# Kernel tuning notes

Hardware: AMD Instinct MI355X
Metric: run time of the kernel (lower is better)

The kernel has to match this reference:

```python
import jax, jax.numpy as jnp
import numpy as np

B, N, C, M, OUT = 4, 256, 32, 4, 64


def _uniform(k, shape, fan_in):
    s = 1.0 / np.sqrt(fan_in)
    return jax.random.uniform(k, shape, jnp.float32, -s, s)


def setup_inputs() -> dict:
    key = jax.random.key(0)
    ks = jax.random.split(key, 11)
    return {
        "x": jax.random.normal(ks[0], (B, N, N, C), jnp.float32),
        # Neighborhood / SnConv2to1 linears (in=C, out=M neighborhood channels)
        "w1_nb": _uniform(ks[1], (3 * C, M), 3 * C),
        "b1_nb": _uniform(ks[2], (M,), 3 * C),
        "w0_nb": _uniform(ks[3], (2 * C, M), 2 * C),
        "b0_nb": _uniform(ks[4], (M,), 2 * C),
        # SnConv2 linears (in channels = M*C after neighborhood product)
        "w2d": _uniform(ks[5], (2 * M * C, OUT), 2 * M * C),
        "b2d": _uniform(ks[6], (OUT,), 2 * M * C),
        "w1d": _uniform(ks[7], (3 * M * C, OUT), 3 * M * C),
        "b1d": _uniform(ks[8], (OUT,), 3 * M * C),
        "w0d": _uniform(ks[9], (2 * M * C, OUT), 2 * M * C),
        "b0d": _uniform(ks[10], (OUT,), 2 * M * C),
    }


def _contractions(x):
    # x: [B, n, n, c]; mask=None, reduction='mean' path of _get_contractions
    n = x.shape[1]
    rowsum = x.sum(axis=1) / n                      # [B, n, c]
    colsum = x.sum(axis=2) / n                      # [B, n, c]
    diag = jnp.diagonal(x, axis1=1, axis2=2)        # [B, c, n]
    rowcolsum = x.sum(axis=(1, 2)) / (n * n)        # [B, c]
    diag_sum = diag.sum(axis=-1) / n                # [B, c]  (/= sqrt(n^2))
    diag = jnp.moveaxis(diag, -1, 1)                # move_from_end -> [B, n, c]
    return rowsum, colsum, diag, rowcolsum, diag_sum


def reference(x, w1_nb, b1_nb, w0_nb, b0_nb, w2d, b2d, w1d, b1d, w0d, b0d):
    # ---- Neighborhood: SnConv2to1 -> sigmoid ----
    rs, cs, dg, rcs, ds = _contractions(x)
    obj1 = jnp.concatenate([rs, cs, dg], axis=-1)             # [B, n, 3C]
    obj0 = jnp.concatenate([rcs, ds], axis=-1)                # [B, 2C]
    node = obj1 @ w1_nb + b1_nb + (obj0 @ w0_nb + b0_nb)[:, None, :]
    neighbs = jax.nn.sigmoid(node)                            # [B, n, M]
    # ---- _neighbor_elementwise_product ----
    expanded = neighbs[:, None, :, :] * neighbs[:, :, None, :]  # [B, n, n, M]
    # channel_product: outer product over channel dims, collapsed to M*C
    xl = (expanded[..., :, None] * x[..., None, :]).reshape(B, N, N, M * C)
    # ---- SnConv2 on the localized tensor ----
    rs2, cs2, dg2, rcs2, ds2 = _contractions(xl)
    obj2d = jnp.concatenate([xl, jnp.swapaxes(xl, 1, 2)], axis=-1)  # [B,n,n,2MC]
    obj1d = jnp.concatenate([rs2, cs2, dg2], axis=-1)               # [B,n,3MC]
    obj0d = jnp.concatenate([rcs2, ds2], axis=-1)                   # [B,2MC]
    out = (obj2d @ w2d + b2d
           + (obj1d @ w1d + b1d)[:, None, :, :]
           + (obj0d @ w0d + b0d)[:, None, None, :])                 # [B,n,n,OUT]
    return out
```

## Files before the change

### kernel.cpp

```cpp
#include <hip/hip_runtime.h>
#include <math.h>

#define Bv 4
#define Nv 256
#define Cv 32
#define Mv 4
#define OUTv 64
#define MCv (Mv*Cv)

typedef _Float16 h8 __attribute__((ext_vector_type(8)));
typedef _Float16 h4 __attribute__((ext_vector_type(4)));
typedef float f4 __attribute__((ext_vector_type(4)));

__device__ __align__(16) float g_rs  [Bv * Nv * Cv];
__device__ __align__(16) float g_cs  [Bv * Nv * Cv];
__device__ __align__(16) float g_dgx [Bv * Nv * Cv];
__device__ __align__(16) float g_nb  [Bv * Nv * Mv];
__device__ __align__(16) float g_S1  [Bv * Nv * MCv];
__device__ __align__(16) float g_S2  [Bv * Nv * MCv];
__device__ __align__(16) float g_rcs2[Bv * MCv];
__device__ __align__(16) float g_ds2 [Bv * MCv];
__device__ __align__(16) float g_t0g [Bv * OUTv];
__device__ __align__(16) float g_addv[Bv * Nv * OUTv];
__device__ __align__(16) _Float16 g_wfrag[8 * 4 * 64 * 8];

__global__ void k_wpackz(const float* __restrict__ w2d) {
    int t = threadIdx.x;
    int r = blockIdx.x;
    if (r == 8) {
        if (t < 128) ((float4*)g_rcs2)[t] = {0.f,0.f,0.f,0.f};
        else         ((float4*)g_ds2)[t - 128] = {0.f,0.f,0.f,0.f};
        return;
    }
    int fi = r * 256 + t;
    int s = fi >> 8, q = (fi >> 6) & 3, lane = fi & 63;
    int k0 = s * 32 + ((lane >> 4) << 3);
    int o = q * 16 + (lane & 15);
    #pragma unroll
    for (int jj = 0; jj < 8; jj++)
        g_wfrag[fi * 8 + jj] = (_Float16)w2d[(size_t)(k0 + jj) * OUTv + o];
}

__global__ __launch_bounds__(256) void k_contract1(const float* __restrict__ x) {
    int bx = blockIdx.x, b = blockIdx.y;
    int t = threadIdx.x, c4 = t & 7, sub = t >> 3;
    const float4* xb4 = (const float4*)(x + (size_t)b * Nv * Nv * Cv);
    __shared__ float red[32][36];
    float4 acc = {0.f,0.f,0.f,0.f};
    if (bx < Nv) {
        int n = bx;
        for (int i = sub; i < Nv; i += 32) {
            float4 v = xb4[((size_t)i * Nv + n) * 8 + c4];
            acc.x += v.x; acc.y += v.y; acc.z += v.z; acc.w += v.w;
        }
        red[sub][c4*4+0] = acc.x; red[sub][c4*4+1] = acc.y;
        red[sub][c4*4+2] = acc.z; red[sub][c4*4+3] = acc.w;
        __syncthreads();
        if (t < 32) {
            float s = 0.f;
            #pragma unroll
            for (int k = 0; k < 32; k++) s += red[k][t];
            g_rs[(b * Nv + n) * Cv + t] = s * (1.0f / Nv);
        }
        if (t < 8) ((float4*)g_dgx)[(b * Nv + n) * 8 + t] = xb4[((size_t)n * Nv + n) * 8 + t];
    } else {
        int n = bx - Nv;
        for (int j = sub; j < Nv; j += 32) {
            float4 v = xb4[((size_t)n * Nv + j) * 8 + c4];
            acc.x += v.x; acc.y += v.y; acc.z += v.z; acc.w += v.w;
        }
        red[sub][c4*4+0] = acc.x; red[sub][c4*4+1] = acc.y;
        red[sub][c4*4+2] = acc.z; red[sub][c4*4+3] = acc.w;
        __syncthreads();
        if (t < 32) {
            float s = 0.f;
            #pragma unroll
            for (int k = 0; k < 32; k++) s += red[k][t];
            g_cs[(b * Nv + n) * Cv + t] = s * (1.0f / Nv);
        }
    }
}

__global__ void k_neighb(const float* __restrict__ w1, const float* __restrict__ b1,
                         const float* __restrict__ w0, const float* __restrict__ b0) {
    int b = blockIdx.x, t = threadIdx.x;
    int c = t & 31, sub = t >> 5;
    float ar = 0.f, ad = 0.f;
    for (int n = sub; n < Nv; n += 8) {
        ar += g_rs[(b * Nv + n) * Cv + c];
        ad += g_dgx[(b * Nv + n) * Cv + c];
    }
    __shared__ float red[8][64];
    __shared__ float obj0[64];
    __shared__ float t0nb[4];
    red[sub][c] = ar;
    red[sub][32 + c] = ad;
    __syncthreads();
    if (t < 64) {
        float s = 0.f;
        #pragma unroll
        for (int k = 0; k < 8; k++) s += red[k][t];
        obj0[t] = s * (1.0f / Nv);
    }
    __syncthreads();
    if (t < 4) {
        float v = b0[t];
        for (int k = 0; k < 2 * Cv; k++) v += obj0[k] * w0[k * Mv + t];
        t0nb[t] = v;
    }
    __syncthreads();
    int n = t;
    float node[4];
    #pragma unroll
    for (int m = 0; m < 4; m++) node[m] = t0nb[m] + b1[m];
    for (int cc = 0; cc < Cv; cc++) {
        float r = g_rs[(b * Nv + n) * Cv + cc];
        float s = g_cs[(b * Nv + n) * Cv + cc];
        float d = g_dgx[(b * Nv + n) * Cv + cc];
        #pragma unroll
        for (int m = 0; m < 4; m++)
            node[m] += r * w1[cc * Mv + m] + s * w1[(Cv + cc) * Mv + m] + d * w1[(2 * Cv + cc) * Mv + m];
    }
    #pragma unroll
    for (int m = 0; m < 4; m++)
        g_nb[(b * Nv + n) * Mv + m] = 1.0f / (1.0f + expf(-node[m]));
}

__global__ __launch_bounds__(256) void k_wsum(const float* __restrict__ x) {
    int bx = blockIdx.x, b = blockIdx.y;
    int t = threadIdx.x, c4 = t & 7, sub = t >> 3;
    __shared__ __align__(16) float4 nbl[Nv];
    if (t < Nv) nbl[t] = ((const float4*)(g_nb + (size_t)b * Nv * Mv))[t];
    __syncthreads();
    const float4* xb4 = (const float4*)(x + (size_t)b * Nv * Nv * Cv);
    float4 a[4];
    #pragma unroll
    for (int m = 0; m < 4; m++) a[m] = {0.f,0.f,0.f,0.f};
    __shared__ float red[32][132];
    if (bx < Nv) {
        int n = bx;
        for (int i = sub; i < Nv; i += 32) {
            float4 v = xb4[((size_t)i * Nv + n) * 8 + c4];
            float4 nv = nbl[i];
            a[0].x += nv.x*v.x; a[0].y += nv.x*v.y; a[0].z += nv.x*v.z; a[0].w += nv.x*v.w;
            a[1].x += nv.y*v.x; a[1].y += nv.y*v.y; a[1].z += nv.y*v.z; a[1].w += nv.y*v.w;
            a[2].x += nv.z*v.x; a[2].y += nv.z*v.y; a[2].z += nv.z*v.z; a[2].w += nv.z*v.w;
            a[3].x += nv.w*v.x; a[3].y += nv.w*v.y; a[3].z += nv.w*v.z; a[3].w += nv.w*v.w;
        }
        #pragma unroll
        for (int m = 0; m < 4; m++) {
            red[sub][m*32 + c4*4+0] = a[m].x; red[sub][m*32 + c4*4+1] = a[m].y;
            red[sub][m*32 + c4*4+2] = a[m].z; red[sub][m*32 + c4*4+3] = a[m].w;
        }
        __syncthreads();
        if (t < 128) {
            float s = 0.f;
            #pragma unroll
            for (int k = 0; k < 32; k++) s += red[k][t];
            g_S1[(size_t)(b * Nv + n) * MCv + t] = s;
            int m = t >> 5, c = t & 31;
            float nv = ((const float*)&nbl[n])[m];
            atomicAdd(&g_rcs2[b * MCv + t], nv * s);
            atomicAdd(&g_ds2 [b * MCv + t], nv * nv * g_dgx[(b * Nv + n) * Cv + c]);
        }
    } else {
        int n = bx - Nv;
        for (int j = sub; j < Nv; j += 32) {
            float4 v = xb4[((size_t)n * Nv + j) * 8 + c4];
            float4 nv = nbl[j];
            a[0].x += nv.x*v.x; a[0].y += nv.x*v.y; a[0].z += nv.x*v.z; a[0].w += nv.x*v.w;
            a[1].x += nv.y*v.x; a[1].y += nv.y*v.y; a[1].z += nv.y*v.z; a[1].w += nv.y*v.w;
            a[2].x += nv.z*v.x; a[2].y += nv.z*v.y; a[2].z += nv.z*v.z; a[2].w += nv.z*v.w;
            a[3].x += nv.w*v.x; a[3].y += nv.w*v.y; a[3].z += nv.w*v.z; a[3].w += nv.w*v.w;
        }
        #pragma unroll
        for (int m = 0; m < 4; m++) {
            red[sub][m*32 + c4*4+0] = a[m].x; red[sub][m*32 + c4*4+1] = a[m].y;
            red[sub][m*32 + c4*4+2] = a[m].z; red[sub][m*32 + c4*4+3] = a[m].w;
        }
        __syncthreads();
        if (t < 128) {
            float s = 0.f;
            #pragma unroll
            for (int k = 0; k < 32; k++) s += red[k][t];
            g_S2[(size_t)(b * Nv + n) * MCv + t] = s;
        }
    }
}

__global__ void k_t0(const float* __restrict__ w0d, const float* __restrict__ b0d) {
    int b = blockIdx.x, t = threadIdx.x;
    __shared__ float rc[MCv], ds[MCv];
    rc[t] = g_rcs2[b * MCv + t] * (1.0f / ((float)Nv * Nv));
    ds[t] = g_ds2 [b * MCv + t] * (1.0f / Nv);
    __syncthreads();
    if (t < OUTv) {
        float v = b0d[t];
        for (int k = 0; k < MCv; k++)
            v += rc[k] * w0d[k * OUTv + t] + ds[k] * w0d[(MCv + k) * OUTv + t];
        g_t0g[b * OUTv + t] = v;
    }
}

__global__ __launch_bounds__(256) void k_add(const float* __restrict__ w1d,
                                             const float* __restrict__ b1d,
                                             const float* __restrict__ b2d) {
    int b = blockIdx.y, n = blockIdx.x;
    int t = threadIdx.x, o = t & 63, ks = t >> 6;
    __shared__ float red[4][64];
    const float invN = 1.0f / Nv;
    float nv = g_nb[(b * Nv + n) * Mv + ks];
    float f = nv * invN, d2 = nv * nv;
    const float* S1r = g_S1 + (size_t)(b * Nv + n) * MCv + ks * 32;
    const float* S2r = g_S2 + (size_t)(b * Nv + n) * MCv + ks * 32;
    const float* dgr = g_dgx + (size_t)(b * Nv + n) * Cv;
    float acc = 0.f;
    #pragma unroll 8
    for (int c = 0; c < 32; c++) {
        int mc = ks * 32 + c;
        acc += f * S1r[c] * w1d[(size_t)mc * OUTv + o]
             + f * S2r[c] * w1d[(size_t)(MCv + mc) * OUTv + o]
             + d2 * dgr[c] * w1d[(size_t)(2 * MCv + mc) * OUTv + o];
    }
    red[ks][o] = acc;
    __syncthreads();
    if (t < 64) {
        float v = red[0][t] + red[1][t] + red[2][t] + red[3][t]
                + b1d[t] + b2d[t] + g_t0g[b * OUTv + t];
        g_addv[(size_t)(b * Nv + n) * OUTv + t] = v;
    }
}

#define XPAD 40
__global__ __launch_bounds__(256) void k_main(const float* __restrict__ x,
                                              float* __restrict__ out) {
    int jt = blockIdx.x, i = blockIdx.y, b = blockIdx.z;
    int j0 = jt * 128;
    int t = threadIdx.x;
    int lane = t & 63, w = t >> 6;
    int rowA = lane & 15, quad = lane >> 4;

    __shared__ __align__(16) _Float16 Wl[8 * 4 * 64 * 8];
    __shared__ __align__(16) _Float16 Xt[128 * XPAD];
    __shared__ __align__(16) _Float16 Xb[128 * XPAD];

    {
        const float4* src = (const float4*)g_wfrag;
        float4* dst = (float4*)Wl;
        #pragma unroll
        for (int r = 0; r < 8; r++) dst[r * 256 + t] = src[r * 256 + t];
    }
    {
        const float4* x4 = (const float4*)x;
        #pragma unroll
        for (int r = 0; r < 4; r++) {
            int idx = r * 256 + t;
            int j = idx >> 3, c4 = idx & 7;
            float4 v = x4[((size_t)(b * Nv + i) * Nv + j0 + j) * 8 + c4];
            h4 hv; hv[0] = (_Float16)v.x; hv[1] = (_Float16)v.y;
            hv[2] = (_Float16)v.z; hv[3] = (_Float16)v.w;
            *(h4*)&Xt[j * XPAD + c4 * 4] = hv;
            float4 u = x4[((size_t)(b * Nv + j0 + j) * Nv + i) * 8 + c4];
            h4 hu; hu[0] = (_Float16)u.x; hu[1] = (_Float16)u.y;
            hu[2] = (_Float16)u.z; hu[3] = (_Float16)u.w;
            *(h4*)&Xb[j * XPAD + c4 * 4] = hu;
        }
    }
    int jl1 = w * 32 + rowA, jl2 = jl1 + 16;
    _Float16 e1h[4], e2h[4];
    {
        const float* ni = g_nb + (size_t)(b * Nv + i) * Mv;
        const float* n1 = g_nb + (size_t)(b * Nv + j0 + jl1) * Mv;
        const float* n2 = g_nb + (size_t)(b * Nv + j0 + jl2) * Mv;
        #pragma unroll
        for (int m = 0; m < 4; m++) {
            e1h[m] = (_Float16)(ni[m] * n1[m]);
            e2h[m] = (_Float16)(ni[m] * n2[m]);
        }
    }
    __syncthreads();

    f4 acc[2][4];
    #pragma unroll
    for (int js = 0; js < 2; js++)
        #pragma unroll
        for (int q = 0; q < 4; q++) acc[js][q] = {0.f, 0.f, 0.f, 0.f};

    const h8* Wf = (const h8*)Wl;
    #pragma unroll
    for (int part = 0; part < 2; part++) {
        const _Float16* X = part ? Xb : Xt;
        h8 xv1 = *(const h8*)&X[jl1 * XPAD + quad * 8];
        h8 xv2 = *(const h8*)&X[jl2 * XPAD + quad * 8];
        #pragma unroll
        for (int m = 0; m < 4; m++) {
            h8 a1 = xv1 * e1h[m];
            h8 a2 = xv2 * e2h[m];
            int s = part * 4 + m;
            #pragma unroll
            for (int q = 0; q < 4; q++) {
                h8 bf = Wf[(s * 4 + q) * 64 + lane];
                acc[0][q] = __builtin_amdgcn_mfma_f32_16x16x32_f16(a1, bf, acc[0][q], 0, 0, 0);
                acc[1][q] = __builtin_amdgcn_mfma_f32_16x16x32_f16(a2, bf, acc[1][q], 0, 0, 0);
            }
        }
    }
    #pragma unroll
    for (int js = 0; js < 2; js++) {
        int jbase = j0 + w * 32 + js * 16 + quad * 4;
        #pragma unroll
        for (int q = 0; q < 4; q++) {
            int o = q * 16 + rowA;
            #pragma unroll
            for (int r = 0; r < 4; r++) {
                int j = jbase + r;
                float v = acc[js][q][r] + g_addv[(size_t)(b * Nv + j) * OUTv + o];
                out[(((size_t)(b * Nv + i)) * Nv + j) * OUTv + o] = v;
            }
        }
    }
}

extern "C" void kernel_launch(void* const* d_in, const int* in_sizes, int n_in,
                              void* d_out, int out_size, void* d_ws, size_t ws_size,
                              hipStream_t stream) {
    const float* x     = (const float*)d_in[0];
    const float* w1_nb = (const float*)d_in[1];
    const float* b1_nb = (const float*)d_in[2];
    const float* w0_nb = (const float*)d_in[3];
    const float* b0_nb = (const float*)d_in[4];
    const float* w2d   = (const float*)d_in[5];
    const float* b2d   = (const float*)d_in[6];
    const float* w1d   = (const float*)d_in[7];
    const float* b1d   = (const float*)d_in[8];
    const float* w0d   = (const float*)d_in[9];
    const float* b0d   = (const float*)d_in[10];
    float* out = (float*)d_out;
    (void)d_ws; (void)ws_size;

    hipLaunchKernelGGL(k_wpackz, dim3(9), dim3(256), 0, stream, w2d);
    hipLaunchKernelGGL(k_contract1, dim3(2 * Nv, Bv), dim3(256), 0, stream, x);
    hipLaunchKernelGGL(k_neighb, dim3(Bv), dim3(256), 0, stream,
                       w1_nb, b1_nb, w0_nb, b0_nb);
    hipLaunchKernelGGL(k_wsum, dim3(2 * Nv, Bv), dim3(256), 0, stream, x);
    hipLaunchKernelGGL(k_t0, dim3(Bv), dim3(128), 0, stream, w0d, b0d);
    hipLaunchKernelGGL(k_add, dim3(Nv, Bv), dim3(256), 0, stream,
                       w1d, b1d, b2d);
    hipLaunchKernelGGL(k_main, dim3(2, Nv, Bv), dim3(256), 0, stream, x, out);
}
```

Baseline: 185.1 us.

## Fuse small kernels, parallelize neighborhood, tile main kernel over multiple rows

The obj0 reduction moves into k_contract1 via atomics. k_neighb is spread over more blocks with a split channel reduction, and k_t0 is folded into k_add. k_main now handles ITILE rows of i per block, so the weight-fragment LDS staging, the addv row loads and the neighbour loads are reused across rows, and outputs use nontemporal stores. This cuts launch count and redundant per-block setup, at the cost of fewer blocks in k_main, float atomics that make summation order nondeterministic, and a redundant w0d computation in every k_add block.

```diff
diff --git a/kernel.cpp b/kernel.cpp
--- a/kernel.cpp
+++ b/kernel.cpp
@@ -7,6 +7,7 @@
 #define Mv 4
 #define OUTv 64
 #define MCv (Mv*Cv)
+#define ITILE 4
 
 typedef _Float16 h8 __attribute__((ext_vector_type(8)));
 typedef _Float16 h4 __attribute__((ext_vector_type(4)));
@@ -18,9 +19,9 @@
 __device__ __align__(16) float g_nb  [Bv * Nv * Mv];
 __device__ __align__(16) float g_S1  [Bv * Nv * MCv];
 __device__ __align__(16) float g_S2  [Bv * Nv * MCv];
+__device__ __align__(16) float g_obj0[Bv * 64];
 __device__ __align__(16) float g_rcs2[Bv * MCv];
 __device__ __align__(16) float g_ds2 [Bv * MCv];
-__device__ __align__(16) float g_t0g [Bv * OUTv];
 __device__ __align__(16) float g_addv[Bv * Nv * OUTv];
 __device__ __align__(16) _Float16 g_wfrag[8 * 4 * 64 * 8];
 
@@ -30,6 +31,7 @@
     if (r == 8) {
         if (t < 128) ((float4*)g_rcs2)[t] = {0.f,0.f,0.f,0.f};
         else         ((float4*)g_ds2)[t - 128] = {0.f,0.f,0.f,0.f};
+        if (t < 64)  ((float4*)g_obj0)[t] = {0.f,0.f,0.f,0.f};
         return;
     }
     int fi = r * 256 + t;
@@ -47,6 +49,7 @@
     const float4* xb4 = (const float4*)(x + (size_t)b * Nv * Nv * Cv);
     __shared__ float red[32][36];
     float4 acc = {0.f,0.f,0.f,0.f};
+    const float invN = 1.0f / Nv;
     if (bx < Nv) {
         int n = bx;
         for (int i = sub; i < Nv; i += 32) {
@@ -60,9 +63,18 @@
             float s = 0.f;
             #pragma unroll
             for (int k = 0; k < 32; k++) s += red[k][t];
-            g_rs[(b * Nv + n) * Cv + t] = s * (1.0f / Nv);
-        }
-        if (t < 8) ((float4*)g_dgx)[(b * Nv + n) * 8 + t] = xb4[((size_t)n * Nv + n) * 8 + t];
+            s *= invN;
+            g_rs[(b * Nv + n) * Cv + t] = s;
+            atomicAdd(&g_obj0[b * 64 + t], s * invN);
+        }
+        if (t < 8) {
+            float4 v = xb4[((size_t)n * Nv + n) * 8 + t];
+            ((float4*)g_dgx)[(b * Nv + n) * 8 + t] = v;
+            atomicAdd(&g_obj0[b * 64 + 32 + t*4 + 0], v.x * invN);
+            atomicAdd(&g_obj0[b * 64 + 32 + t*4 + 1], v.y * invN);
+            atomicAdd(&g_obj0[b * 64 + 32 + t*4 + 2], v.z * invN);
+            atomicAdd(&g_obj0[b * 64 + 32 + t*4 + 3], v.w * invN);
+        }
     } else {
         int n = bx - Nv;
         for (int j = sub; j < Nv; j += 32) {
@@ -76,54 +88,53 @@
             float s = 0.f;
             #pragma unroll
             for (int k = 0; k < 32; k++) s += red[k][t];
-            g_cs[(b * Nv + n) * Cv + t] = s * (1.0f / Nv);
-        }
-    }
-}
-
-__global__ void k_neighb(const float* __restrict__ w1, const float* __restrict__ b1,
-                         const float* __restrict__ w0, const float* __restrict__ b0) {
-    int b = blockIdx.x, t = threadIdx.x;
-    int c = t & 31, sub = t >> 5;
-    float ar = 0.f, ad = 0.f;
-    for (int n = sub; n < Nv; n += 8) {
-        ar += g_rs[(b * Nv + n) * Cv + c];
-        ad += g_dgx[(b * Nv + n) * Cv + c];
-    }
-    __shared__ float red[8][64];
-    __shared__ float obj0[64];
-    __shared__ float t0nb[4];
-    red[sub][c] = ar;
-    red[sub][32 + c] = ad;
-    __syncthreads();
-    if (t < 64) {
-        float s = 0.f;
-        #pragma unroll
-        for (int k = 0; k < 8; k++) s += red[k][t];
-        obj0[t] = s * (1.0f / Nv);
-    }
+            g_cs[(b * Nv + n) * Cv + t] = s * invN;
+        }
+    }
+}
+
+__global__ __launch_bounds__(256) void k_neighb(const float* __restrict__ w1,
+                                                const float* __restrict__ b1,
+                                                const float* __restrict__ w0,
+                                                const float* __restrict__ b0) {
+    int ng = blockIdx.x, b = blockIdx.y;
+    int t = threadIdx.x;
+    __shared__ float obj0[64], t0nb[4];
+    if (t < 64) obj0[t] = g_obj0[b * 64 + t];
     __syncthreads();
     if (t < 4) {
         float v = b0[t];
-        for (int k = 0; k < 2 * Cv; k++) v += obj0[k] * w0[k * Mv + t];
+        for (int k = 0; k < 64; k++) v += obj0[k] * w0[k * Mv + t];
         t0nb[t] = v;
     }
+    int n = ng * 64 + (t >> 2), part = t & 3;
+    float node[4] = {0.f, 0.f, 0.f, 0.f};
+    const float* rsr = g_rs  + (size_t)(b * Nv + n) * Cv;
+    const float* csr = g_cs  + (size_t)(b * Nv + n) * Cv;
+    const float* dgr = g_dgx + (size_t)(b * Nv + n) * Cv;
+    #pragma unroll
+    for (int q = 0; q < 8; q++) {
+        int cc = part * 8 + q;
+        float r = rsr[cc], s = csr[cc], d = dgr[cc];
+        #pragma unroll
+        for (int m = 0; m < 4; m++)
+            node[m] += r * w1[cc * Mv + m] + s * w1[(Cv + cc) * Mv + m]
+                     + d * w1[(2 * Cv + cc) * Mv + m];
+    }
+    __shared__ float red[256][4];
+    #pragma unroll
+    for (int m = 0; m < 4; m++) red[t][m] = node[m];
     __syncthreads();
-    int n = t;
-    float node[4];
-    #pragma unroll
-    for (int m = 0; m < 4; m++) node[m] = t0nb[m] + b1[m];
-    for (int cc = 0; cc < Cv; cc++) {
-        float r = g_rs[(b * Nv + n) * Cv + cc];
-        float s = g_cs[(b * Nv + n) * Cv + cc];
-        float d = g_dgx[(b * Nv + n) * Cv + cc];
-        #pragma unroll
-        for (int m = 0; m < 4; m++)
-            node[m] += r * w1[cc * Mv + m] + s * w1[(Cv + cc) * Mv + m] + d * w1[(2 * Cv + cc) * Mv + m];
-    }
-    #pragma unroll
-    for (int m = 0; m < 4; m++)
-        g_nb[(b * Nv + n) * Mv + m] = 1.0f / (1.0f + expf(-node[m]));
+    if (part == 0) {
+        float4 o4;
+        #pragma unroll
+        for (int m = 0; m < 4; m++) {
+            float v = t0nb[m] + b1[m]
+                    + red[t][m] + red[t+1][m] + red[t+2][m] + red[t+3][m];
+            ((float*)&o4)[m] = 1.0f / (1.0f + expf(-v));
+        }
+        ((float4*)g_nb)[b * Nv + n] = o4;
+    }
 }
 
 __global__ __launch_bounds__(256) void k_wsum(const float* __restrict__ x) {
@@ -188,33 +199,29 @@
     }
 }
 
-__global__ void k_t0(const float* __restrict__ w0d, const float* __restrict__ b0d) {
-    int b = blockIdx.x, t = threadIdx.x;
-    __shared__ float rc[MCv], ds[MCv];
-    rc[t] = g_rcs2[b * MCv + t] * (1.0f / ((float)Nv * Nv));
-    ds[t] = g_ds2 [b * MCv + t] * (1.0f / Nv);
-    __syncthreads();
-    if (t < OUTv) {
-        float v = b0d[t];
-        for (int k = 0; k < MCv; k++)
-            v += rc[k] * w0d[k * OUTv + t] + ds[k] * w0d[(MCv + k) * OUTv + t];
-        g_t0g[b * OUTv + t] = v;
-    }
-}
-
 __global__ __launch_bounds__(256) void k_add(const float* __restrict__ w1d,
                                              const float* __restrict__ b1d,
-                                             const float* __restrict__ b2d) {
+                                             const float* __restrict__ b2d,
+                                             const float* __restrict__ w0d,
+                                             const float* __restrict__ b0d) {
     int b = blockIdx.y, n = blockIdx.x;
     int t = threadIdx.x, o = t & 63, ks = t >> 6;
     __shared__ float red[4][64];
     const float invN = 1.0f / Nv;
+    const float invN2 = 1.0f / ((float)Nv * Nv);
+    float acc = 0.f;
+    #pragma unroll 8
+    for (int c = 0; c < 32; c++) {
+        int k = ks * 32 + c;
+        float rc = g_rcs2[b * MCv + k] * invN2;
+        float dv = g_ds2 [b * MCv + k] * invN;
+        acc += rc * w0d[(size_t)k * OUTv + o] + dv * w0d[(size_t)(MCv + k) * OUTv + o];
+    }
     float nv = g_nb[(b * Nv + n) * Mv + ks];
     float f = nv * invN, d2 = nv * nv;
     const float* S1r = g_S1 + (size_t)(b * Nv + n) * MCv + ks * 32;
     const float* S2r = g_S2 + (size_t)(b * Nv + n) * MCv + ks * 32;
     const float* dgr = g_dgx + (size_t)(b * Nv + n) * Cv;
-    float acc = 0.f;
     #pragma unroll 8
     for (int c = 0; c < 32; c++) {
         int mc = ks * 32 + c;
@@ -226,7 +233,7 @@
     __syncthreads();
     if (t < 64) {
         float v = red[0][t] + red[1][t] + red[2][t] + red[3][t]
-                + b1d[t] + b2d[t] + g_t0g[b * OUTv + t];
+                + b1d[t] + b2d[t] + b0d[t];
         g_addv[(size_t)(b * Nv + n) * OUTv + t] = v;
     }
 }
@@ -234,8 +241,8 @@
 #define XPAD 40
 __global__ __launch_bounds__(256) void k_main(const float* __restrict__ x,
                                               float* __restrict__ out) {
-    int jt = blockIdx.x, i = blockIdx.y, b = blockIdx.z;
-    int j0 = jt * 128;
+    int jt = blockIdx.x, ib = blockIdx.y, b = blockIdx.z;
+    int j0 = jt * 128, i0 = ib * ITILE;
     int t = threadIdx.x;
     int lane = t & 63, w = t >> 6;
     int rowA = lane & 15, quad = lane >> 4;
@@ -250,8 +257,24 @@
         #pragma unroll
         for (int r = 0; r < 8; r++) dst[r * 256 + t] = src[r * 256 + t];
     }
-    {
-        const float4* x4 = (const float4*)x;
+    int jl1 = w * 32 + rowA, jl2 = jl1 + 16;
+    float av[2][4][4];
+    #pragma unroll
+    for (int js = 0; js < 2; js++) {
+        int jb = j0 + w * 32 + js * 16 + quad * 4;
+        #pragma unroll
+        for (int q = 0; q < 4; q++)
+            #pragma unroll
+            for (int r = 0; r < 4; r++)
+                av[js][q][r] = g_addv[(size_t)(b * Nv + jb + r) * OUTv + q * 16 + rowA];
+    }
+    float4 nj1 = ((const float4*)g_nb)[b * Nv + j0 + jl1];
+    float4 nj2 = ((const float4*)g_nb)[b * Nv + j0 + jl2];
+    const float4* x4 = (const float4*)x;
+    const h8* Wf = (const h8*)Wl;
+
+    for (int ii = 0; ii < ITILE; ii++) {
+        int i = i0 + ii;
         #pragma unroll
         for (int r = 0; r < 4; r++) {
             int idx = r * 256 + t;
@@ -265,59 +288,55 @@
             hu[2] = (_Float16)u.z; hu[3] = (_Float16)u.w;
             *(h4*)&Xb[j * XPAD + c4 * 4] = hu;
         }
-    }
-    int jl1 = w * 32 + rowA, jl2 = jl1 + 16;
-    _Float16 e1h[4], e2h[4];
-    {
-        const float* ni = g_nb + (size_t)(b * Nv + i) * Mv;
-        const float* n1 = g_nb + (size_t)(b * Nv + j0 + jl1) * Mv;
-        const float* n2 = g_nb + (size_t)(b * Nv + j0 + jl2) * Mv;
+        float4 ni = ((const float4*)g_nb)[b * Nv + i];
+        _Float16 e1h[4], e2h[4];
         #pragma unroll
         for (int m = 0; m < 4; m++) {
-            e1h[m] = (_Float16)(ni[m] * n1[m]);
-            e2h[m] = (_Float16)(ni[m] * n2[m]);
-        }
-    }
-    __syncthreads();
-
-    f4 acc[2][4];
-    #pragma unroll
-    for (int js = 0; js < 2; js++)
-        #pragma unroll
-        for (int q = 0; q < 4; q++) acc[js][q] = {0.f, 0.f, 0.f, 0.f};
-
-    const h8* Wf = (const h8*)Wl;
-    #pragma unroll
-    for (int part = 0; part < 2; part++) {
-        const _Float16* X = part ? Xb : Xt;
-        h8 xv1 = *(const h8*)&X[jl1 * XPAD + quad * 8];
-        h8 xv2 = *(const h8*)&X[jl2 * XPAD + quad * 8];
-        #pragma unroll
-        for (int m = 0; m < 4; m++) {
-            h8 a1 = xv1 * e1h[m];
-            h8 a2 = xv2 * e2h[m];
-            int s = part * 4 + m;
+            e1h[m] = (_Float16)(((const float*)&ni)[m] * ((const float*)&nj1)[m]);
+            e2h[m] = (_Float16)(((const float*)&ni)[m] * ((const float*)&nj2)[m]);
+        }
+        __syncthreads();
+
+        f4 acc[2][4];
+        #pragma unroll
+        for (int js = 0; js < 2; js++)
+            #pragma unroll
+            for (int q = 0; q < 4; q++) acc[js][q] = {0.f, 0.f, 0.f, 0.f};
+
+        #pragma unroll
+        for (int part = 0; part < 2; part++) {
+            const _Float16* X = part ? Xb : Xt;
+            h8 xv1 = *(const h8*)&X[jl1 * XPAD + quad * 8];
+            h8 xv2 = *(const h8*)&X[jl2 * XPAD + quad * 8];
+            #pragma unroll
+            for (int m = 0; m < 4; m++) {
+                h8 a1 = xv1 * e1h[m];
+                h8 a2 = xv2 * e2h[m];
+                int s = part * 4 + m;
+                #pragma unroll
+                for (int q = 0; q < 4; q++) {
+                    h8 bf = Wf[(s * 4 + q) * 64 + lane];
+                    acc[0][q] = __builtin_amdgcn_mfma_f32_16x16x32_f16(a1, bf, acc[0][q], 0, 0, 0);
+                    acc[1][q] = __builtin_amdgcn_mfma_f32_16x16x32_f16(a2, bf, acc[1][q], 0, 0, 0);
+                }
+            }
+        }
+        #pragma unroll
+        for (int js = 0; js < 2; js++) {
+            int jbase = j0 + w * 32 + js * 16 + quad * 4;
             #pragma unroll
             for (int q = 0; q < 4; q++) {
-                h8 bf = Wf[(s * 4 + q) * 64 + lane];
-                acc[0][q] = __builtin_amdgcn_mfma_f32_16x16x32_f16(a1, bf, acc[0][q], 0, 0, 0);
-                acc[1][q] = __builtin_amdgcn_mfma_f32_16x16x32_f16(a2, bf, acc[1][q], 0, 0, 0);
+                int o = q * 16 + rowA;
+                #pragma unroll
+                for (int r = 0; r < 4; r++) {
+                    int j = jbase + r;
+                    float v = acc[js][q][r] + av[js][q][r];
+                    __builtin_nontemporal_store(v,
+                        &out[(((size_t)(b * Nv + i)) * Nv + j) * OUTv + o]);
+                }
             }
         }
-    }
-    #pragma unroll
-    for (int js = 0; js < 2; js++) {
-        int jbase = j0 + w * 32 + js * 16 + quad * 4;
-        #pragma unroll
-        for (int q = 0; q < 4; q++) {
-            int o = q * 16 + rowA;
-            #pragma unroll
-            for (int r = 0; r < 4; r++) {
-                int j = jbase + r;
-                float v = acc[js][q][r] + g_addv[(size_t)(b * Nv + j) * OUTv + o];
-                out[(((size_t)(b * Nv + i)) * Nv + j) * OUTv + o] = v;
-            }
-        }
+        __syncthreads();
     }
 }
 
@@ -340,11 +359,10 @@
 
     hipLaunchKernelGGL(k_wpackz, dim3(9), dim3(256), 0, stream, w2d);
     hipLaunchKernelGGL(k_contract1, dim3(2 * Nv, Bv), dim3(256), 0, stream, x);
-    hipLaunchKernelGGL(k_neighb, dim3(Bv), dim3(256), 0, stream,
+    hipLaunchKernelGGL(k_neighb, dim3(Nv / 64, Bv), dim3(256), 0, stream,
                        w1_nb, b1_nb, w0_nb, b0_nb);
     hipLaunchKernelGGL(k_wsum, dim3(2 * Nv, Bv), dim3(256), 0, stream, x);
-    hipLaunchKernelGGL(k_t0, dim3(Bv), dim3(128), 0, stream, w0d, b0d);
     hipLaunchKernelGGL(k_add, dim3(Nv, Bv), dim3(256), 0, stream,
-                       w1d, b1d, b2d);
-    hipLaunchKernelGGL(k_main, dim3(2, Nv, Bv), dim3(256), 0, stream, x, out);
-}
+                       w1d, b1d, b2d, w0d, b0d);
+    hipLaunchKernelGGL(k_main, dim3(2, Nv / ITILE, Bv), dim3(256), 0, stream, x, out);
+}
```

Result: slower. 209.0 us (+13.0%).
